# Optimization experiments

Measured on AMD Instinct MI355X. Metric: run time of the kernel, lower is better.

The kernel has to match this reference:

```python
import jax, jax.numpy as jnp
import numpy as np

MAX_SLOTS = 8192


def _compress_lowest_importance_pair(x):
    """Vectorized version of the per-batch python loop: merge the adjacent pair
    with the lowest summed L2-norm into one averaged slot. [B,S,d] -> [B,S-1,d]."""
    B, S, d = x.shape
    imp = jnp.linalg.norm(x, axis=-1)              # [B, S]
    pair_scores = imp[:, :-1] + imp[:, 1:]          # [B, S-1]
    p = jnp.argmin(pair_scores, axis=1)             # [B] merge index per row
    idx = jnp.arange(S - 1)                         # output slot positions
    # gather: out[j] = x[j] for j<=p, x[j+1] for j>p
    g = idx[None, :] + (idx[None, :] > p[:, None]).astype(idx.dtype)  # [B, S-1]
    out = jnp.take_along_axis(x, g[:, :, None], axis=1)               # [B, S-1, d]
    left = jnp.take_along_axis(x, p[:, None, None], axis=1)           # [B, 1, d]
    right = jnp.take_along_axis(x, (p + 1)[:, None, None], axis=1)    # [B, 1, d]
    merged = 0.5 * (left + right)
    # overwrite position p with the merged slot
    out = jnp.where(idx[None, :, None] == p[:, None, None], merged, out)
    return out


def _compress_oldest_pair(x):
    merged = 0.5 * (x[:, :1, :] + x[:, 1:2, :])
    return jnp.concatenate([merged, x[:, 2:, :]], axis=1)


def setup_inputs() -> dict:
    key = jax.random.key(0)
    k1, k2 = jax.random.split(key)
    bank_states = jax.random.normal(k1, (16, 8192, 512), dtype=jnp.float32)
    refresh_states = jax.random.normal(k2, (16, 32, 512), dtype=jnp.float32)
    return {"bank_states": bank_states, "refresh_states": refresh_states}


def reference(bank_states, refresh_states):
    # write(): refresh_states.detach(); sizes here take the concat+compress path
    refresh = jax.lax.stop_gradient(refresh_states)
    updated = jnp.concatenate([bank_states, refresh], axis=1)  # [B, S_bank+S_ref, d]
    # shapes are static, so this python while unrolls a fixed number of steps
    while updated.shape[1] > MAX_SLOTS:
        if updated.shape[1] <= 2:
            updated = _compress_oldest_pair(updated)
        else:
            updated = _compress_lowest_importance_pair(updated)
    return updated
```

## Files before the change

### kernel.cpp

```cpp
#include <hip/hip_runtime.h>
#include <cstdint>
#include <cstddef>

#define B_DIM  16
#define S_BANK 8192
#define S_REF  32
#define S_TOT  8224
#define NMERGE 32
#define D      512
#define NCH    129

typedef float vfloat4 __attribute__((ext_vector_type(4)));
typedef unsigned long long u64;
#define DEADPK 0xFFFFFFFFFFFFFFFFULL

__device__ __forceinline__ int d_lo(double d){ union{double d; int i[2];}u; u.d=d; return u.i[0]; }
__device__ __forceinline__ int d_hi(double d){ union{double d; int i[2];}u; u.d=d; return u.i[1]; }
__device__ __forceinline__ double d_mk(int hi,int lo){ union{double d; int i[2];}u; u.i[0]=lo;u.i[1]=hi; return u.d; }
__device__ __forceinline__ int u_lo(u64 v){ return (int)(v & 0xFFFFFFFFULL); }
__device__ __forceinline__ int u_hi(u64 v){ return (int)(v >> 32); }
__device__ __forceinline__ u64 u_mk(int hi,int lo){ return ((u64)(unsigned)hi << 32) | (u64)(unsigned)lo; }
__device__ __forceinline__ u64 d_bits(double d){ union{double d; u64 u;}x; x.d=d; return x.u; }

__device__ __forceinline__ u64 pack_score(double s, int j) {
    return (d_bits(s) & ~0x3FFFULL) | (u64)(unsigned)j;
}

template<int CTRL, int ROWM>
__device__ __forceinline__ u64 dpp_u64(u64 v) {
    int lo = __builtin_amdgcn_update_dpp(u_lo(v), u_lo(v), CTRL, ROWM, 0xF, false);
    int hi = __builtin_amdgcn_update_dpp(u_hi(v), u_hi(v), CTRL, ROWM, 0xF, false);
    return u_mk(hi, lo);
}
__device__ __forceinline__ u64 rl_u64(u64 v, int l) {
    int lo = __builtin_amdgcn_readlane(u_lo(v), l);
    int hi = __builtin_amdgcn_readlane(u_hi(v), l);
    return u_mk(hi, lo);
}
__device__ __forceinline__ u64 lexmin_wave_u64(u64 v) {
    u64 w;
    w = dpp_u64<0x111,0xF>(v); if (w < v) v = w;
    w = dpp_u64<0x112,0xF>(v); if (w < v) v = w;
    w = dpp_u64<0x114,0xF>(v); if (w < v) v = w;
    w = dpp_u64<0x118,0xF>(v); if (w < v) v = w;
    w = dpp_u64<0x142,0xF>(v); if (w < v) v = w;
    w = dpp_u64<0x143,0xF>(v); if (w < v) v = w;
    return rl_u64(v, 63);
}
__device__ __forceinline__ u64 scan_min_incl(u64 v) {
    u64 w;
    w = dpp_u64<0x111,0xF>(v); if (w < v) v = w;
    w = dpp_u64<0x112,0xF>(v); if (w < v) v = w;
    w = dpp_u64<0x114,0xF>(v); if (w < v) v = w;
    w = dpp_u64<0x118,0xF>(v); if (w < v) v = w;
    w = dpp_u64<0x142,0xA>(v); if (w < v) v = w;
    w = dpp_u64<0x143,0xC>(v); if (w < v) v = w;
    return v;
}
__device__ __forceinline__ u64 scan_min_suffix(u64 v, int lane) {
    u64 w;
    w = dpp_u64<0x101,0xF>(v); if (w < v) v = w;
    w = dpp_u64<0x102,0xF>(v); if (w < v) v = w;
    w = dpp_u64<0x104,0xF>(v); if (w < v) v = w;
    w = dpp_u64<0x108,0xF>(v); if (w < v) v = w;
    u64 t16 = rl_u64(v, 16), t32 = rl_u64(v, 32), t48 = rl_u64(v, 48);
    u64 s3 = t48;
    u64 s2 = (t32 < s3) ? t32 : s3;
    u64 s1 = (t16 < s2) ? t16 : s2;
    int row = lane >> 4;
    u64 add = (row == 0) ? s1 : (row == 1) ? s2 : (row == 2) ? s3 : DEADPK;
    if (add < v) v = add;
    return v;
}
template<int CTRL>
__device__ __forceinline__ void sum_level(double& v) {
    int lo2 = __builtin_amdgcn_update_dpp(0, d_lo(v), CTRL, 0xF, 0xF, true);
    int hi2 = __builtin_amdgcn_update_dpp(0, d_hi(v), CTRL, 0xF, 0xF, true);
    v += d_mk(hi2, lo2);
}
__device__ __forceinline__ double sum_wave(double v) {
    sum_level<0x111>(v); sum_level<0x112>(v); sum_level<0x114>(v);
    sum_level<0x118>(v); sum_level<0x142>(v); sum_level<0x143>(v);
    int lo = __builtin_amdgcn_readlane(d_lo(v), 63);
    int hi = __builtin_amdgcn_readlane(d_hi(v), 63);
    return d_mk(hi, lo);
}

__global__ __launch_bounds__(256) void norms_kernel(const float* __restrict__ bank,
                                                    const float* __restrict__ refresh,
                                                    double* __restrict__ norms) {
    int gw_lin = (int)((blockIdx.x * 256 + threadIdx.x) >> 6);
    int gw   = B_DIM * S_TOT - 1 - gw_lin;
    int lane = threadIdx.x & 63;
    int b = gw / S_TOT;
    int s = gw - b * S_TOT;
    const float4* src = (const float4*)(s < S_BANK
        ? bank    + ((size_t)b * S_BANK + s) * D
        : refresh + ((size_t)b * S_REF + (s - S_BANK)) * D);
    float4 f0 = src[lane];
    float4 f1 = src[lane + 64];
    double acc = 0.0;
    acc += (double)f0.x * f0.x + (double)f0.y * f0.y + (double)f0.z * f0.z + (double)f0.w * f0.w;
    acc += (double)f1.x * f1.x + (double)f1.y * f1.y + (double)f1.z * f1.z + (double)f1.w * f1.w;
    acc = sum_wave(acc);
    if (lane == 0) norms[gw] = sqrt(acc);
}

__global__ __launch_bounds__(256) void chunkmin_kernel(const double* __restrict__ norms,
                                                       u64* __restrict__ c_pk_g) {
    int w    = (int)((blockIdx.x * 256 + threadIdx.x) >> 6);
    int lane = threadIdx.x & 63;
    if (w >= B_DIM * NCH) return;
    int b = w / NCH;
    int c = w - b * NCH;
    int j = c * 64 + lane;
    u64 pk = DEADPK;
    if (j <= S_TOT - 2) {
        double a = norms[b * S_TOT + j];
        double d = norms[b * S_TOT + j + 1];
        pk = pack_score(a + d, j);
    }
    pk = lexmin_wave_u64(pk);
    if (lane == 0) c_pk_g[b * NCH + c] = pk;
}

__device__ __forceinline__ const float* slot_gptr(int id, int b,
        const float* bank, const float* refresh) {
    return (id < S_BANK) ? bank    + ((size_t)b * S_BANK + id) * D
                         : refresh + ((size_t)b * S_REF + (id - S_BANK)) * D;
}

#define NBULK (B_DIM * 4096)

__global__ __launch_bounds__(256) void fused_kernel(const float* __restrict__ bank,
        const float* __restrict__ refresh, const double* __restrict__ norms,
        const u64* __restrict__ c_pk_g, int* __restrict__ flag_g,
        vfloat4* __restrict__ out) {
    __shared__ double s_wimp[194];
    __shared__ u64    c_pk[NCH];
    __shared__ u64    pref[192], suf[192];
    __shared__ int    rec_L[NMERGE], rec_R[NMERGE];
    __shared__ u64    rec_chosen[NMERGE];
    __shared__ u64    s_PL, s_SR;
    __shared__ int    s_flag;
    __shared__ int    sh_p0;

    const int t    = threadIdx.x;
    const int lane = t & 63;
    const int wid  = t >> 6;
    const double INF = __builtin_inf();

    if (blockIdx.x >= 16) {
        int e  = blockIdx.x - 16;
        int b  = e >> 12;
        int pr = (e & 4095) << 1;
        if (wid == 0) {
            u64 a  = (lane < NCH) ? c_pk_g[b * NCH + lane] : DEADPK;
            u64 b2 = (lane + 64 < NCH) ? c_pk_g[b * NCH + lane + 64] : DEADPK;
            u64 m = (a < b2) ? a : b2;
            u64 c2 = (lane == 0) ? c_pk_g[b * NCH + 128] : DEADPK;
            m = (m < c2) ? m : c2;
            m = lexmin_wave_u64(m);
            if (lane == 0) sh_p0 = (int)(m & 0x3FFFULL);
        }
        __syncthreads();
        const int p0 = sh_p0;
        int r = pr + (t >> 7);
        int c = t & 127;
        int s = -1;
        if (r < p0 - 31)      s = r;
        else if (r > p0)      s = r + 32;
        if (s >= 0) {
            const vfloat4* sp = (const vfloat4*)slot_gptr(s, b, bank, refresh);
            vfloat4 v = sp[c];
            __builtin_nontemporal_store(v, &out[((size_t)b * S_BANK + r) * (D / 4) + c]);
        }
        return;
    }

    const int b = blockIdx.x;

    if (t < NCH) c_pk[t] = c_pk_g[b * NCH + t];
    __syncthreads();

    u64 pk_min0;
    {
        u64 a = c_pk[lane];
        u64 bq = c_pk[lane + 64];
        u64 c = (lane == 0) ? c_pk[128] : DEADPK;
        u64 m = (a < bq) ? a : bq;
        m = (m < c) ? m : c;
        pk_min0 = lexmin_wave_u64(m);
    }
    const int p0 = (int)(pk_min0 & 0x3FFFULL);

    const int cmid = p0 >> 6;
    int wsx = cmid - 1;
    if (wsx < 0) wsx = 0;
    if (wsx > NCH - 3) wsx = NCH - 3;
    const int ws  = wsx;
    const int wlo = ws * 64;

    for (int j = t; j < 194; j += 256) {
        int g = wlo + j;
        if (g < S_TOT) s_wimp[j] = norms[b * S_TOT + g];
    }
    __syncthreads();

    float4 m0r, m1r;

    if (wid == 0) {
        const float4* gA = (const float4*)slot_gptr(p0, b, bank, refresh);
        const float4* gB = (const float4*)slot_gptr(p0 + 1, b, bank, refresh);
        float4 a0 = gA[2 * lane], a1 = gA[2 * lane + 1];
        float4 b0 = gB[2 * lane], b1 = gB[2 * lane + 1];
        int q;
        q = (p0 - 1 >= 0) ? p0 - 1 : 0;
        const float4* gq = (const float4*)slot_gptr(q, b, bank, refresh);
        float4 cL0 = gq[2 * lane], cL1 = gq[2 * lane + 1];
        q = (p0 + 2 <= S_TOT - 1) ? p0 + 2 : S_TOT - 1;
        gq = (const float4*)slot_gptr(q, b, bank, refresh);
        float4 cR0 = gq[2 * lane], cR1 = gq[2 * lane + 1];
        q = (p0 - 2 >= 0) ? p0 - 2 : 0;
        gq = (const float4*)slot_gptr(q, b, bank, refresh);
        float4 fL0 = gq[2 * lane], fL1 = gq[2 * lane + 1];
        q = (p0 + 3 <= S_TOT - 1) ? p0 + 3 : S_TOT - 1;
        gq = (const float4*)slot_gptr(q, b, bank, refresh);
        float4 fR0 = gq[2 * lane], fR1 = gq[2 * lane + 1];

        m0r.x = 0.5f * (a0.x + b0.x); m0r.y = 0.5f * (a0.y + b0.y);
        m0r.z = 0.5f * (a0.z + b0.z); m0r.w = 0.5f * (a0.w + b0.w);
        m1r.x = 0.5f * (a1.x + b1.x); m1r.y = 0.5f * (a1.y + b1.y);
        m1r.z = 0.5f * (a1.z + b1.z); m1r.w = 0.5f * (a1.w + b1.w);
        double ss = 0.0;
        ss += (double)m0r.x * m0r.x + (double)m0r.y * m0r.y + (double)m0r.z * m0r.z + (double)m0r.w * m0r.w;
        ss += (double)m1r.x * m1r.x + (double)m1r.y * m1r.y + (double)m1r.z * m1r.z + (double)m1r.w * m1r.w;
        double nrm = sqrt(sum_wave(ss));
        int L = p0, R = p0 + 1;
        if (t == 0) { rec_L[0] = L; rec_R[0] = R; rec_chosen[0] = pk_min0; }

        for (int step = 1; step < NMERGE; ++step) {
            const int cl = L - 1, cr = R + 1;
            const bool hasL = (cl >= 0);
            const bool hasR = (cr < S_TOT);
            const double il = hasL ? s_wimp[cl - wlo] : INF;
            const double ir = hasR ? s_wimp[cr - wlo] : INF;
            const u64 pkL = hasL ? pack_score(il + nrm, cl) : DEADPK;
            const u64 pkR = hasR ? pack_score(nrm + ir, L)  : DEADPK;
            const bool goL = (pkL < pkR);
            const u64 chosen = goL ? pkL : pkR;
            float4 a0s, a1s, b0s, b1s;
            if (goL) { a0s = cL0; a1s = cL1; b0s = m0r; b1s = m1r; }
            else     { a0s = m0r; a1s = m1r; b0s = cR0; b1s = cR1; }
            m0r.x = 0.5f * (a0s.x + b0s.x); m0r.y = 0.5f * (a0s.y + b0s.y);
            m0r.z = 0.5f * (a0s.z + b0s.z); m0r.w = 0.5f * (a0s.w + b0s.w);
            m1r.x = 0.5f * (a1s.x + b1s.x); m1r.y = 0.5f * (a1s.y + b1s.y);
            m1r.z = 0.5f * (a1s.z + b1s.z); m1r.w = 0.5f * (a1s.w + b1s.w);
            if (goL) {
                L = cl;
                cL0 = fL0; cL1 = fL1;
                int nq = (L - 2 >= 0) ? L - 2 : 0;
                const float4* gp = (const float4*)slot_gptr(nq, b, bank, refresh);
                fL0 = gp[2 * lane]; fL1 = gp[2 * lane + 1];
            } else {
                R = cr;
                cR0 = fR0; cR1 = fR1;
                int nq = (R + 2 <= S_TOT - 1) ? R + 2 : S_TOT - 1;
                const float4* gp = (const float4*)slot_gptr(nq, b, bank, refresh);
                fR0 = gp[2 * lane]; fR1 = gp[2 * lane + 1];
            }
            double ss2 = 0.0;
            ss2 += (double)m0r.x * m0r.x + (double)m0r.y * m0r.y + (double)m0r.z * m0r.z + (double)m0r.w * m0r.w;
            ss2 += (double)m1r.x * m1r.x + (double)m1r.y * m1r.y + (double)m1r.z * m1r.z + (double)m1r.w * m1r.w;
            nrm = sqrt(sum_wave(ss2));
            if (t == 0) { rec_L[step] = L; rec_R[step] = R; rec_chosen[step] = chosen; }
        }
    } else {
        int c = ws + (wid - 1);
        int idx = c * 64 + lane;
        u64 pk0 = (idx <= S_TOT - 2)
                    ? pack_score(s_wimp[idx - wlo] + s_wimp[idx + 1 - wlo], idx)
                    : DEADPK;
        pref[idx - wlo] = scan_min_incl(pk0);
        suf[idx - wlo]  = scan_min_suffix(pk0, lane);
        if (wid == 1) {
            u64 x0 = (lane < ws) ? c_pk[lane] : DEADPK;
            u64 x1 = (lane + 64 < ws) ? c_pk[lane + 64] : DEADPK;
            u64 pl = (x0 < x1) ? x0 : x1;
            pl = lexmin_wave_u64(pl);
            if (lane == 0) s_PL = pl;
        }
        if (wid == 2) {
            u64 y0 = (lane > ws + 2) ? c_pk[lane] : DEADPK;
            u64 y1 = (lane + 64 > ws + 2) ? c_pk[lane + 64] : DEADPK;
            u64 y2 = (lane == 0 && 128 > ws + 2) ? c_pk[128] : DEADPK;
            u64 sr = (y0 < y1) ? y0 : y1;
            sr = (sr < y2) ? sr : y2;
            sr = lexmin_wave_u64(sr);
            if (lane == 0) s_SR = sr;
        }
    }
    __syncthreads();

    if (wid == 0) {
        u64 cf0 = pref[63], cf1 = pref[127];
        u64 sf1 = suf[64],  sf2 = suf[128];
        u64 PL = s_PL, SR = s_SR;
        bool ok = true;
        if (lane >= 1 && lane < NMERGE) {
            int Lp = rec_L[lane - 1], Rp = rec_R[lane - 1];
            int q1 = Lp - 2 - wlo;
            u64 ol = DEADPK;
            if (q1 >= 0) {
                ol = pref[q1];
                int r1 = q1 >> 6;
                if (r1 >= 1 && cf0 < ol) ol = cf0;
                if (r1 >= 2 && cf1 < ol) ol = cf1;
            }
            if (PL < ol) ol = PL;
            int q2 = Rp + 1 - wlo;
            u64 orr = suf[q2];
            int r2 = q2 >> 6;
            if (r2 <= 0 && sf1 < orr) orr = sf1;
            if (r2 <= 1 && sf2 < orr) orr = sf2;
            if (SR < orr) orr = SR;
            u64 O = (ol < orr) ? ol : orr;
            ok = rec_chosen[lane] < O;
        }
        if (lane == 0) ok = ok && (rec_R[NMERGE - 1] - rec_L[NMERGE - 1] == NMERGE);
        unsigned long long bad = __ballot(!ok);
        if (lane == 0) s_flag = (bad != 0ULL) ? 1 : 0;
    }
    __syncthreads();

    if (t == 0) flag_g[b] = s_flag;
    if (s_flag != 0) return;

    const int Ls = rec_L[NMERGE - 1];
    if (wid == 0) {
        vfloat4 v0, v1;
        v0.x = m0r.x; v0.y = m0r.y; v0.z = m0r.z; v0.w = m0r.w;
        v1.x = m1r.x; v1.y = m1r.y; v1.z = m1r.z; v1.w = m1r.w;
        __builtin_nontemporal_store(v0, &out[((size_t)b * S_BANK + Ls) * (D / 4) + 2 * lane]);
        __builtin_nontemporal_store(v1, &out[((size_t)b * S_BANK + Ls) * (D / 4) + 2 * lane + 1]);
    }
    const int lo = (p0 - 31 > 0) ? p0 - 31 : 0;
    const int hi = (p0 < S_BANK - 1) ? p0 : S_BANK - 1;
    for (int r = lo + wid; r <= hi; r += 4) {
        if (r == Ls) continue;
        int s = (r < Ls) ? r : r + 32;
        const vfloat4* sp = (const vfloat4*)slot_gptr(s, b, bank, refresh);
        vfloat4 v0 = sp[2 * lane], v1 = sp[2 * lane + 1];
        __builtin_nontemporal_store(v0, &out[((size_t)b * S_BANK + r) * (D / 4) + 2 * lane]);
        __builtin_nontemporal_store(v1, &out[((size_t)b * S_BANK + r) * (D / 4) + 2 * lane + 1]);
    }
}

struct FallLds {
    unsigned short s_next[S_TOT];
    float          s_mvec[NMERGE][D];
    unsigned short s_mpos[NMERGE];
    unsigned short s_dead[NMERGE];
};

__global__ __launch_bounds__(256) void fallback_kernel(const float* __restrict__ bank,
        const float* __restrict__ refresh, const double* __restrict__ norms,
        const u64* __restrict__ c_pk_g, const int* __restrict__ flag_g,
        unsigned short* __restrict__ idx_out, vfloat4* __restrict__ out) {
    const int b = blockIdx.x;
    if (flag_g[b] == 0) return;

    __shared__ double  s_imp[S_TOT];
    __shared__ u64     c_pk[NCH];
    __shared__ FallLds G;

    const int t    = threadIdx.x;
    const int lane = t & 63;
    const int wid  = t >> 6;
    const double INF = __builtin_inf();

    if (t < NCH) c_pk[t] = c_pk_g[b * NCH + t];
    for (int j = t; j < S_TOT; j += 256) {
        s_imp[j] = norms[b * S_TOT + j];
        G.s_next[j] = (unsigned short)((j + 1 < S_TOT) ? (j + 1) : 0xFFFF);
    }
    __syncthreads();

    if (wid == 0) {
        u64 cv0 = c_pk[lane];
        u64 cv1 = c_pk[lane + 64];
        u64 cv2 = (lane == 0) ? c_pk[128] : DEADPK;

        int mpos_reg = -1;
        int prev_p = -1, prev_pv = -1, prev_nk = -1;
        int pvok = 0, nkok = 0;
        float4 mm0, mm1, pva0, pva1, pnk0, pnk1;

        for (int step = 0; step < NMERGE; ++step) {
            u64 m = (cv0 < cv1) ? cv0 : cv1;
            m = (m < cv2) ? m : cv2;
            m = lexmin_wave_u64(m);
            const int p = (int)(m & 0x3FFFULL);

            const bool hitA = pvok && (p == prev_pv);
            const bool hitB = nkok && (p == prev_p);

            int k, nk;
            float4 a0, a1, b0, b1;
            if (hitA) {
                k = prev_p; nk = prev_nk;
                a0 = pva0; a1 = pva1; b0 = mm0; b1 = mm1;
            } else if (hitB) {
                k = prev_nk; nk = G.s_next[k];
                a0 = mm0; a1 = mm1; b0 = pnk0; b1 = pnk1;
            } else {
                k = G.s_next[p]; nk = G.s_next[k];
                unsigned long long bA = __ballot((lane < step) && (mpos_reg == p));
                const int ia = bA ? (S_TOT + 63 - __clzll(bA)) : p;
                unsigned long long bB = __ballot((lane < step) && (mpos_reg == k));
                const int ib = bB ? (S_TOT + 63 - __clzll(bB)) : k;
                if (ia < S_TOT) { const float4* g = (const float4*)slot_gptr(ia, b, bank, refresh);
                                  a0 = g[2 * lane]; a1 = g[2 * lane + 1]; }
                else            { const float4* g = (const float4*)&G.s_mvec[ia - S_TOT][0];
                                  a0 = g[2 * lane]; a1 = g[2 * lane + 1]; }
                if (ib < S_TOT) { const float4* g = (const float4*)slot_gptr(ib, b, bank, refresh);
                                  b0 = g[2 * lane]; b1 = g[2 * lane + 1]; }
                else            { const float4* g = (const float4*)&G.s_mvec[ib - S_TOT][0];
                                  b0 = g[2 * lane]; b1 = g[2 * lane + 1]; }
            }

            int pv;
            if (hitB) {
                pv = prev_pv;
            } else {
                int jq = p - 1 - lane;
                bool plive = (jq >= 0) && (s_imp[jq] < 1e300);
                unsigned long long pb = __ballot(plive);
                pv = pb ? (p - __ffsll((unsigned long long)pb)) : -1;
            }

            const double imp_nk = s_imp[(nk != 0xFFFF) ? nk : 0];
            const double imp_pv = s_imp[(pv >= 0) ? pv : 0];
            const int chp = p >> 6, chk = k >> 6;
            const int chv = (pv >= 0) ? (pv >> 6) : -1;
            const int csB = (chk != chp) ? chk : -1;
            const int csC = (chv >= 0 && chv != chp && chv != chk) ? chv : -1;
            const int jjA = chp * 64 + lane;
            const bool validA = (jjA < S_TOT) && (jjA != k);
            const int rawNxtA = validA ? (int)G.s_next[jjA] : 0xFFFF;
            const double impA = validA ? s_imp[jjA] : INF;
            const int nxtA = (jjA == p) ? nk : rawNxtA;
            const double impNxtA = (nxtA != 0xFFFF) ? s_imp[nxtA] : INF;

            float4 m0, m1;
            m0.x = 0.5f * (a0.x + b0.x); m0.y = 0.5f * (a0.y + b0.y);
            m0.z = 0.5f * (a0.z + b0.z); m0.w = 0.5f * (a0.w + b0.w);
            m1.x = 0.5f * (a1.x + b1.x); m1.y = 0.5f * (a1.y + b1.y);
            m1.z = 0.5f * (a1.z + b1.z); m1.w = 0.5f * (a1.w + b1.w);
            {
                float4* dst = (float4*)&G.s_mvec[step][0];
                dst[2 * lane] = m0; dst[2 * lane + 1] = m1;
            }
            if (lane == step) mpos_reg = p;

            if (step + 1 < NMERGE) {
                prev_p = p; prev_pv = pv; prev_nk = nk;
                mm0 = m0; mm1 = m1;
                pvok = (pv >= 0); nkok = (nk != 0xFFFF);
                unsigned long long bpv = __ballot((lane <= step) && (mpos_reg == pv));
                const int ipv = bpv ? (S_TOT + 63 - __clzll(bpv)) : pv;
                unsigned long long bnk = __ballot((lane <= step) && (mpos_reg == nk));
                const int ink = bnk ? (S_TOT + 63 - __clzll(bnk)) : nk;
                if (pvok) {
                    if (ipv < S_TOT) { const float4* g = (const float4*)slot_gptr(ipv, b, bank, refresh);
                                       pva0 = g[2 * lane]; pva1 = g[2 * lane + 1]; }
                    else             { const float4* g = (const float4*)&G.s_mvec[ipv - S_TOT][0];
                                       pva0 = g[2 * lane]; pva1 = g[2 * lane + 1]; }
                }
                if (nkok) {
                    if (ink < S_TOT) { const float4* g = (const float4*)slot_gptr(ink, b, bank, refresh);
                                       pnk0 = g[2 * lane]; pnk1 = g[2 * lane + 1]; }
                    else             { const float4* g = (const float4*)&G.s_mvec[ink - S_TOT][0];
                                       pnk0 = g[2 * lane]; pnk1 = g[2 * lane + 1]; }
                }
            }

            double ss = 0.0;
            ss += (double)m0.x * m0.x + (double)m0.y * m0.y + (double)m0.z * m0.z + (double)m0.w * m0.w;
            ss += (double)m1.x * m1.x + (double)m1.y * m1.y + (double)m1.z * m1.z + (double)m1.w * m1.w;
            const double nrm = sqrt(sum_wave(ss));

            if (lane == 0) {
                G.s_next[p]    = (unsigned short)nk;
                s_imp[k]       = INF;
                s_imp[p]       = nrm;
                G.s_mpos[step] = (unsigned short)p;
                G.s_dead[step] = (unsigned short)k;
            }

            {
                u64 sc = DEADPK;
                if (validA && nxtA != 0xFFFF) {
                    double a0d = (jjA == p) ? nrm : impA;
                    if (a0d < 1e300) {
                        double a1d = (nxtA == p) ? nrm : impNxtA;
                        sc = pack_score(a0d + a1d, jjA);
                    }
                }
                sc = lexmin_wave_u64(sc);
                if (chp < 64)       { if (lane == chp)      cv0 = sc; }
                else if (chp < 128) { if (lane == chp - 64) cv1 = sc; }
                else                { if (lane == 0)        cv2 = sc; }
            }
            if (csB >= 0) {
                int jj = csB * 64 + lane;
                u64 sc = DEADPK;
                if (jj < S_TOT && jj != k) {
                    int nxt = (int)G.s_next[jj];
                    if (nxt != 0xFFFF) {
                        double a0d = s_imp[jj];
                        if (a0d < 1e300) sc = pack_score(a0d + s_imp[nxt], jj);
                    }
                }
                sc = lexmin_wave_u64(sc);
                if (csB < 64)       { if (lane == csB)      cv0 = sc; }
                else if (csB < 128) { if (lane == csB - 64) cv1 = sc; }
                else                { if (lane == 0)        cv2 = sc; }
            }
            if (csC >= 0) {
                int jj = csC * 64 + lane;
                u64 sc = DEADPK;
                if (jj < S_TOT && jj != k) {
                    int nxt = (int)G.s_next[jj];
                    if (nxt != 0xFFFF) {
                        double a0d = s_imp[jj];
                        if (a0d < 1e300) sc = pack_score(a0d + s_imp[nxt], jj);
                    }
                }
                sc = lexmin_wave_u64(sc);
                if (csC < 64)       { if (lane == csC)      cv0 = sc; }
                else if (csC < 128) { if (lane == csC - 64) cv1 = sc; }
                else                { if (lane == 0)        cv2 = sc; }
            }
        }
    }
    __syncthreads();

    for (int j = t; j < S_TOT; j += 256) G.s_next[j] = 0xFFFF;
    __syncthreads();
    if (t == 0)
        for (int m2 = 0; m2 < NMERGE; ++m2) G.s_next[G.s_mpos[m2]] = (unsigned short)m2;
    __syncthreads();
    for (int j = t; j < S_TOT; j += 256) {
        if (s_imp[j] < 1e300) {
            int r = j;
            #pragma unroll
            for (int m2 = 0; m2 < NMERGE; ++m2) r -= (G.s_dead[m2] < j) ? 1 : 0;
            unsigned short lut = G.s_next[j];
            idx_out[b * S_BANK + r] = (lut != 0xFFFF) ? (unsigned short)(S_TOT + lut)
                                                      : (unsigned short)j;
        }
    }
    __syncthreads();

    for (int w = t; w < S_BANK * (D / 4); w += 256) {
        int r = w >> 7, c = w & 127;
        int src = idx_out[b * S_BANK + r];
        vfloat4 v;
        if (src < S_TOT) {
            const vfloat4* sp = (const vfloat4*)slot_gptr(src, b, bank, refresh);
            v = sp[c];
        } else {
            const vfloat4* sp = (const vfloat4*)&G.s_mvec[src - S_TOT][0];
            v = sp[c];
        }
        __builtin_nontemporal_store(v, &out[((size_t)b * S_BANK + r) * (D / 4) + c]);
    }
}

extern "C" void kernel_launch(void* const* d_in, const int* in_sizes, int n_in,
                              void* d_out, int out_size, void* d_ws, size_t ws_size,
                              hipStream_t stream) {
    const float* bank    = (const float*)d_in[0];
    const float* refresh = (const float*)d_in[1];

    double*         norms  = (double*)d_ws;
    u64*            c_pk_g = (u64*)((char*)d_ws + (size_t)B_DIM * S_TOT * sizeof(double));
    int*            flag_g = (int*)((char*)c_pk_g + (size_t)B_DIM * NCH * sizeof(u64));
    unsigned short* idx    = (unsigned short*)((char*)flag_g + 64 * sizeof(int));
    vfloat4*        out    = (vfloat4*)d_out;

    norms_kernel<<<(B_DIM * S_TOT) / 4, 256, 0, stream>>>(bank, refresh, norms);
    chunkmin_kernel<<<(B_DIM * NCH * 64 + 255) / 256, 256, 0, stream>>>(norms, c_pk_g);
    fused_kernel<<<16 + NBULK, 256, 0, stream>>>(bank, refresh, norms, c_pk_g, flag_g, out);
    fallback_kernel<<<B_DIM, 256, 0, stream>>>(bank, refresh, norms, c_pk_g, flag_g, idx, out);
}
```

Measured before the change: 131.2 us.

## Fuse norm and chunk-min kernels and precompute per-batch argmin via atomicMin

The separate norms and chunkmin kernels are merged into one kernel. Each block computes the 65 row norms for one 64-slot chunk into shared memory, reduces the chunk's packed pair-score minimum, and folds it into a per-batch global minimum with atomicMin. The fused and bulk-copy blocks then read the precomputed per-batch merge index directly, instead of each reducing all 129 chunk minima. This removes one launch, the global-memory round trip of norms into chunkmin, and a redundant reduction plus barrier in about 65K bulk blocks. In exchange it adds a memset launch and far fewer waves in flight during the norm pass, each issuing 16 or 17 row loads serially, which may weaken latency hiding.

```diff
diff --git a/kernel.cpp b/kernel.cpp
--- a/kernel.cpp
+++ b/kernel.cpp
@@ -86,56 +86,59 @@
     return d_mk(hi, lo);
 }
 
-__global__ __launch_bounds__(256) void norms_kernel(const float* __restrict__ bank,
-                                                    const float* __restrict__ refresh,
-                                                    double* __restrict__ norms) {
-    int gw_lin = (int)((blockIdx.x * 256 + threadIdx.x) >> 6);
-    int gw   = B_DIM * S_TOT - 1 - gw_lin;
-    int lane = threadIdx.x & 63;
-    int b = gw / S_TOT;
-    int s = gw - b * S_TOT;
-    const float4* src = (const float4*)(s < S_BANK
-        ? bank    + ((size_t)b * S_BANK + s) * D
-        : refresh + ((size_t)b * S_REF + (s - S_BANK)) * D);
-    float4 f0 = src[lane];
-    float4 f1 = src[lane + 64];
-    double acc = 0.0;
-    acc += (double)f0.x * f0.x + (double)f0.y * f0.y + (double)f0.z * f0.z + (double)f0.w * f0.w;
-    acc += (double)f1.x * f1.x + (double)f1.y * f1.y + (double)f1.z * f1.z + (double)f1.w * f1.w;
-    acc = sum_wave(acc);
-    if (lane == 0) norms[gw] = sqrt(acc);
-}
-
-__global__ __launch_bounds__(256) void chunkmin_kernel(const double* __restrict__ norms,
-                                                       u64* __restrict__ c_pk_g) {
-    int w    = (int)((blockIdx.x * 256 + threadIdx.x) >> 6);
-    int lane = threadIdx.x & 63;
-    if (w >= B_DIM * NCH) return;
-    int b = w / NCH;
-    int c = w - b * NCH;
-    int j = c * 64 + lane;
-    u64 pk = DEADPK;
-    if (j <= S_TOT - 2) {
-        double a = norms[b * S_TOT + j];
-        double d = norms[b * S_TOT + j + 1];
-        pk = pack_score(a + d, j);
-    }
-    pk = lexmin_wave_u64(pk);
-    if (lane == 0) c_pk_g[b * NCH + c] = pk;
-}
-
 __device__ __forceinline__ const float* slot_gptr(int id, int b,
         const float* bank, const float* refresh) {
     return (id < S_BANK) ? bank    + ((size_t)b * S_BANK + id) * D
                          : refresh + ((size_t)b * S_REF + (id - S_BANK)) * D;
 }
 
+__global__ __launch_bounds__(256) void normchunk_kernel(const float* __restrict__ bank,
+        const float* __restrict__ refresh, double* __restrict__ norms,
+        u64* __restrict__ c_pk_g, u64* __restrict__ p0pk_g) {
+    __shared__ double s_n[65];
+    const int gb = B_DIM * NCH - 1 - (int)blockIdx.x;
+    const int b = gb / NCH;
+    const int c = gb - b * NCH;
+    const int t = threadIdx.x, lane = t & 63, wid = t >> 6;
+    const int base = c * 64;
+    const int niter = (wid == 3) ? 17 : 16;
+    for (int i = 0; i < niter; ++i) {
+        int s = base + wid * 16 + i;
+        if (s >= S_TOT) break;
+        const float4* src = (const float4*)(s < S_BANK
+            ? bank    + ((size_t)b * S_BANK + s) * D
+            : refresh + ((size_t)b * S_REF + (s - S_BANK)) * D);
+        float4 f0 = src[lane];
+        float4 f1 = src[lane + 64];
+        double acc = 0.0;
+        acc += (double)f0.x * f0.x + (double)f0.y * f0.y + (double)f0.z * f0.z + (double)f0.w * f0.w;
+        acc += (double)f1.x * f1.x + (double)f1.y * f1.y + (double)f1.z * f1.z + (double)f1.w * f1.w;
+        acc = sum_wave(acc);
+        double nv = sqrt(acc);
+        if (lane == 0) {
+            s_n[s - base] = nv;
+            if (i < 16) norms[b * S_TOT + s] = nv;
+        }
+    }
+    __syncthreads();
+    if (wid == 0) {
+        int j = base + lane;
+        u64 pk = DEADPK;
+        if (j <= S_TOT - 2) pk = pack_score(s_n[lane] + s_n[lane + 1], j);
+        pk = lexmin_wave_u64(pk);
+        if (lane == 0) {
+            c_pk_g[b * NCH + c] = pk;
+            atomicMin(p0pk_g + b, pk);
+        }
+    }
+}
+
 #define NBULK (B_DIM * 4096)
 
 __global__ __launch_bounds__(256) void fused_kernel(const float* __restrict__ bank,
         const float* __restrict__ refresh, const double* __restrict__ norms,
-        const u64* __restrict__ c_pk_g, int* __restrict__ flag_g,
-        vfloat4* __restrict__ out) {
+        const u64* __restrict__ c_pk_g, const u64* __restrict__ p0pk_g,
+        int* __restrict__ flag_g, vfloat4* __restrict__ out) {
     __shared__ double s_wimp[194];
     __shared__ u64    c_pk[NCH];
     __shared__ u64    pref[192], suf[192];
@@ -143,7 +146,6 @@
     __shared__ u64    rec_chosen[NMERGE];
     __shared__ u64    s_PL, s_SR;
     __shared__ int    s_flag;
-    __shared__ int    sh_p0;
 
     const int t    = threadIdx.x;
     const int lane = t & 63;
@@ -154,17 +156,7 @@
         int e  = blockIdx.x - 16;
         int b  = e >> 12;
         int pr = (e & 4095) << 1;
-        if (wid == 0) {
-            u64 a  = (lane < NCH) ? c_pk_g[b * NCH + lane] : DEADPK;
-            u64 b2 = (lane + 64 < NCH) ? c_pk_g[b * NCH + lane + 64] : DEADPK;
-            u64 m = (a < b2) ? a : b2;
-            u64 c2 = (lane == 0) ? c_pk_g[b * NCH + 128] : DEADPK;
-            m = (m < c2) ? m : c2;
-            m = lexmin_wave_u64(m);
-            if (lane == 0) sh_p0 = (int)(m & 0x3FFFULL);
-        }
-        __syncthreads();
-        const int p0 = sh_p0;
+        const int p0 = (int)(p0pk_g[b] & 0x3FFFULL);
         int r = pr + (t >> 7);
         int c = t & 127;
         int s = -1;
@@ -181,17 +173,7 @@
     const int b = blockIdx.x;
 
     if (t < NCH) c_pk[t] = c_pk_g[b * NCH + t];
-    __syncthreads();
-
-    u64 pk_min0;
-    {
-        u64 a = c_pk[lane];
-        u64 bq = c_pk[lane + 64];
-        u64 c = (lane == 0) ? c_pk[128] : DEADPK;
-        u64 m = (a < bq) ? a : bq;
-        m = (m < c) ? m : c;
-        pk_min0 = lexmin_wave_u64(m);
-    }
+    const u64 pk_min0 = p0pk_g[b];
     const int p0 = (int)(pk_min0 & 0x3FFFULL);
 
     const int cmid = p0 >> 6;
@@ -586,12 +568,13 @@
 
     double*         norms  = (double*)d_ws;
     u64*            c_pk_g = (u64*)((char*)d_ws + (size_t)B_DIM * S_TOT * sizeof(double));
-    int*            flag_g = (int*)((char*)c_pk_g + (size_t)B_DIM * NCH * sizeof(u64));
+    u64*            p0pk_g = (u64*)((char*)c_pk_g + (size_t)B_DIM * NCH * sizeof(u64));
+    int*            flag_g = (int*)((char*)p0pk_g + B_DIM * sizeof(u64));
     unsigned short* idx    = (unsigned short*)((char*)flag_g + 64 * sizeof(int));
     vfloat4*        out    = (vfloat4*)d_out;
 
-    norms_kernel<<<(B_DIM * S_TOT) / 4, 256, 0, stream>>>(bank, refresh, norms);
-    chunkmin_kernel<<<(B_DIM * NCH * 64 + 255) / 256, 256, 0, stream>>>(norms, c_pk_g);
-    fused_kernel<<<16 + NBULK, 256, 0, stream>>>(bank, refresh, norms, c_pk_g, flag_g, out);
+    hipMemsetAsync(p0pk_g, 0xFF, B_DIM * sizeof(u64), stream);
+    normchunk_kernel<<<B_DIM * NCH, 256, 0, stream>>>(bank, refresh, norms, c_pk_g, p0pk_g);
+    fused_kernel<<<16 + NBULK, 256, 0, stream>>>(bank, refresh, norms, c_pk_g, p0pk_g, flag_g, out);
     fallback_kernel<<<B_DIM, 256, 0, stream>>>(bank, refresh, norms, c_pk_g, flag_g, idx, out);
 }
```

Measured after the change: 141.7 us. 1.08x slower.
